# Kernel optimization log

Hardware: AMD Instinct MI355X
Metric: run time of the kernel (lower is better)

## Reference

```python
import jax, jax.numpy as jnp
import numpy as np

B, S, D_IN, D_OUT = 4, 2048, 1024, 1024

def setup_inputs() -> dict:
    key = jax.random.key(0)
    ks = jax.random.split(key, 6)
    s = 1.0 / np.sqrt(D_IN)
    return {
        "inputs": jax.random.normal(ks[0], (B, S, D_IN), dtype=jnp.float32),
        "Wq": jax.random.normal(ks[1], (D_IN, D_OUT), dtype=jnp.float32) * s,
        "Wk": jax.random.normal(ks[2], (D_IN, D_OUT), dtype=jnp.float32) * s,
        "Wv": jax.random.normal(ks[3], (D_IN, D_OUT), dtype=jnp.float32) * s,
        "Wo": jax.random.normal(ks[4], (D_OUT, D_OUT), dtype=jnp.float32) * (1.0 / np.sqrt(D_OUT)),
        "bo": jax.random.normal(ks[5], (D_OUT,), dtype=jnp.float32) * 0.01,
    }

def reference(inputs, Wq, Wk, Wv, Wo, bo):
    # QKV projections (no bias, matching qkv_bias=False)
    q = inputs @ Wq  # [B,S,D]
    k = inputs @ Wk
    v = inputs @ Wv
    # naive full attention: scores [B,S,S]
    scores = jnp.einsum('bqd,bkd->bqk', q, k) / jnp.sqrt(jnp.asarray(k.shape[-1], q.dtype))
    attn = jax.nn.softmax(scores, axis=-1)
    out = jnp.einsum('bqk,bkd->bqd', attn, v)
    return out @ Wo + bo
```

## Files before the change

kernel.cpp:

```cpp
#include <hip/hip_runtime.h>
#include <hip/hip_bf16.h>
#include <cstdint>

typedef __attribute__((ext_vector_type(8))) __bf16 bf16x8;
typedef __attribute__((ext_vector_type(4))) float  f32x4;

__device__ __forceinline__ unsigned short f2bf(float x) {
    union { float f; unsigned u; } v; v.f = x;
    unsigned r = v.u + 0x7fffu + ((v.u >> 16) & 1u);
    return (unsigned short)(r >> 16);
}
__device__ __forceinline__ unsigned pack2bf(float a, float b) {
    return (unsigned)f2bf(a) | ((unsigned)f2bf(b) << 16);
}

__device__ __forceinline__ void gld_lds16(const unsigned short* g, unsigned short* l) {
    __builtin_amdgcn_global_load_lds(
        (const __attribute__((address_space(1))) unsigned int*)g,
        (__attribute__((address_space(3))) unsigned int*)l,
        16, 0, 0);
}

__global__ void cvt_kernel(const float* __restrict__ in, unsigned short* __restrict__ out, int n4) {
    int i = blockIdx.x * blockDim.x + threadIdx.x;
    if (i < n4) {
        float4 f = ((const float4*)in)[i];
        ushort4 o;
        o.x = f2bf(f.x); o.y = f2bf(f.y); o.z = f2bf(f.z); o.w = f2bf(f.w);
        ((ushort4*)out)[i] = o;
    }
}

__global__ void wpack_kernel(const float* __restrict__ W, unsigned short* __restrict__ out) {
    int tid  = threadIdx.x;
    int lane = tid & 63;
    int chunk = blockIdx.x * 4 + (tid >> 6);
    int nt = chunk >> 5, k32 = chunk & 31;
    int r = lane & 15, q = lane >> 4;
    const float* src = W + (size_t)(k32*32 + q*8) * 1024 + nt*16 + r;
    unsigned o[4];
#pragma unroll
    for (int i = 0; i < 4; i++)
        o[i] = pack2bf(src[(size_t)(2*i) * 1024], src[(size_t)(2*i+1) * 1024]);
    *(uint4*)(out + (size_t)chunk * 512 + lane * 8) = make_uint4(o[0], o[1], o[2], o[3]);
}

__global__ void softmax_kernel(unsigned short* __restrict__ S) {
    const size_t row = blockIdx.x;
    unsigned short* p = S + row * 2048;
    const int tid = threadIdx.x;
    const int wave = tid >> 6, lane = tid & 63;

    uint4 raw = ((const uint4*)p)[tid];
    unsigned u[4] = {raw.x, raw.y, raw.z, raw.w};
    float x[8];
#pragma unroll
    for (int i = 0; i < 4; i++) {
        x[2*i]   = __uint_as_float(u[i] << 16);
        x[2*i+1] = __uint_as_float(u[i] & 0xffff0000u);
    }
    float m = x[0];
#pragma unroll
    for (int i = 1; i < 8; i++) m = fmaxf(m, x[i]);
#pragma unroll
    for (int off = 32; off >= 1; off >>= 1) m = fmaxf(m, __shfl_xor(m, off, 64));
    __shared__ float sm[4], ss[4];
    if (lane == 0) sm[wave] = m;
    __syncthreads();
    m = fmaxf(fmaxf(sm[0], sm[1]), fmaxf(sm[2], sm[3]));

    float e[8], s = 0.f;
#pragma unroll
    for (int i = 0; i < 8; i++) { e[i] = __expf(x[i] - m); s += e[i]; }
#pragma unroll
    for (int off = 32; off >= 1; off >>= 1) s += __shfl_xor(s, off, 64);
    if (lane == 0) ss[wave] = s;
    __syncthreads();
    s = ss[0] + ss[1] + ss[2] + ss[3];
    float inv = 1.0f / s;

    unsigned o[4];
#pragma unroll
    for (int i = 0; i < 4; i++)
        o[i] = pack2bf(e[2*i] * inv, e[2*i+1] * inv);
    ((uint4*)p)[tid] = make_uint4(o[0], o[1], o[2], o[3]);
}

template<int EPI>
__global__ __launch_bounds__(256)
void gemm_pk(const unsigned short* __restrict__ A, const unsigned short* __restrict__ Bpk,
             void* __restrict__ C, unsigned short* __restrict__ Ck, unsigned short* __restrict__ Cv,
             const float* __restrict__ bias,
             int lda, int ldc, int KS, int nk2, float scale,
             long long sA, long long sB, long long sC)
{
    constexpr int SMEM = (EPI == 2) ? 34816 : ((EPI == 1) ? 17408 : 16384);
    __shared__ __align__(16) char smem[SMEM];
    unsigned short* As = (unsigned short*)smem;

    const int tid  = threadIdx.x;
    const int lane = tid & 63;
    const int wave = tid >> 6;
    const int bz = blockIdx.z;
    A   += (size_t)bz * sA;
    Bpk += (size_t)bz * sB;
    const int bm = blockIdx.y * 128;
    const int bn = blockIdx.x * 128;

    const int srow = tid >> 2;
    const int scol = ((tid & 3) ^ ((tid >> 3) & 3)) * 8;
    const unsigned short* pa0 = A + (size_t)(bm + srow) * lda + scol;
    const unsigned short* pa1 = pa0 + 32;
    const unsigned short* pa2 = A + (size_t)(bm + 64 + srow) * lda + scol;
    const unsigned short* pa3 = pa2 + 32;

    const int wm = (wave & 1) * 64;
    const int wn = (wave >> 1) * 64;
    const int ln15 = lane & 15;
    const int quad = lane >> 4;
    const int fko = (quad ^ ((ln15 >> 1) & 3)) * 8;

    const unsigned short* pb[4];
#pragma unroll
    for (int j = 0; j < 4; j++)
        pb[j] = Bpk + (size_t)(((bn + wn + j*16) >> 4) * KS) * 512 + lane * 8;

    f32x4 acc[4][4];
#pragma unroll
    for (int i = 0; i < 4; i++)
#pragma unroll
        for (int j = 0; j < 4; j++) acc[i][j] = (f32x4){0.f, 0.f, 0.f, 0.f};

    const int ldsoff = tid * 16;

    for (int kt = 0; kt < nk2; ++kt) {
        __syncthreads();
        gld_lds16(pa0, (unsigned short*)(smem + ldsoff));
        gld_lds16(pa2, (unsigned short*)(smem + 4096  + ldsoff));
        gld_lds16(pa1, (unsigned short*)(smem + 8192  + ldsoff));
        gld_lds16(pa3, (unsigned short*)(smem + 12288 + ldsoff));
        pa0 += 64; pa1 += 64; pa2 += 64; pa3 += 64;
        bf16x8 b0[4], b1[4];
#pragma unroll
        for (int j = 0; j < 4; j++) {
            b0[j] = *(const bf16x8*)(pb[j]);
            b1[j] = *(const bf16x8*)(pb[j] + 512);
            pb[j] += 1024;
        }
        asm volatile("s_waitcnt vmcnt(0)" ::: "memory");
        __syncthreads();

#pragma unroll
        for (int t = 0; t < 2; t++) {
            bf16x8 af[4];
#pragma unroll
            for (int i = 0; i < 4; i++)
                af[i] = *(const bf16x8*)&As[t*4096 + (wm + i*16 + ln15) * 32 + fko];
#pragma unroll
            for (int i = 0; i < 4; i++)
#pragma unroll
                for (int j = 0; j < 4; j++)
                    acc[i][j] = __builtin_amdgcn_mfma_f32_16x16x32_bf16(
                        af[i], t ? b1[j] : b0[j], acc[i][j], 0, 0, 0);
        }
    }

    if (EPI == 0) {
        float bval[4];
#pragma unroll
        for (int j = 0; j < 4; j++) bval[j] = bias[bn + wn + j*16 + ln15];
        float* Co = (float*)C + (size_t)bz * sC;
#pragma unroll
        for (int i = 0; i < 4; i++) {
            int r0 = bm + wm + i*16 + quad*4;
#pragma unroll
            for (int j = 0; j < 4; j++) {
                int c = bn + wn + j*16 + ln15;
#pragma unroll
                for (int r = 0; r < 4; r++)
                    Co[(size_t)(r0 + r) * ldc + c] = acc[i][j][r] * scale + bval[j];
            }
        }
    } else if (EPI == 1) {
        __syncthreads();
        float* ep = (float*)(smem + wave * 4352);
        unsigned short* Co = (unsigned short*)C + (size_t)bz * sC;
#pragma unroll
        for (int i = 0; i < 4; i++) {
#pragma unroll
            for (int j = 0; j < 4; j++)
#pragma unroll
                for (int r = 0; r < 4; r++)
                    ep[(quad*4 + r) * 68 + j*16 + ln15] = acc[i][j][r] * scale;
            __builtin_amdgcn_s_waitcnt(0);
#pragma unroll
            for (int p = 0; p < 2; p++) {
                int lrow = p*8 + (lane >> 3);
                int col0 = (lane & 7) * 8;
                float4 lo = *(const float4*)&ep[lrow * 68 + col0];
                float4 hi = *(const float4*)&ep[lrow * 68 + col0 + 4];
                uint4 o;
                o.x = pack2bf(lo.x, lo.y); o.y = pack2bf(lo.z, lo.w);
                o.z = pack2bf(hi.x, hi.y); o.w = pack2bf(hi.z, hi.w);
                *(uint4*)&Co[(size_t)(bm + wm + i*16 + lrow) * ldc + bn + wn + col0] = o;
            }
            __builtin_amdgcn_s_waitcnt(0);
        }
    } else {
        __syncthreads();
        float* ep = (float*)(smem + wave * 8704);
        const int region = bn >> 10;
#pragma unroll
        for (int half = 0; half < 2; half++) {
#pragma unroll
            for (int ii = 0; ii < 2; ii++) {
                int i = half*2 + ii;
#pragma unroll
                for (int j = 0; j < 4; j++)
#pragma unroll
                    for (int r = 0; r < 4; r++)
                        ep[(ii*16 + quad*4 + r) * 68 + j*16 + ln15] = acc[i][j][r] * scale;
            }
            __builtin_amdgcn_s_waitcnt(0);
            const int mrow0 = bm + wm + half*32;
            if (region == 0) {
                unsigned short* Q = (unsigned short*)C;
#pragma unroll
                for (int p = 0; p < 4; p++) {
                    int lrow = p*8 + (lane >> 3);
                    int col0 = (lane & 7) * 8;
                    float4 lo = *(const float4*)&ep[lrow * 68 + col0];
                    float4 hi = *(const float4*)&ep[lrow * 68 + col0 + 4];
                    uint4 o;
                    o.x = pack2bf(lo.x, lo.y); o.y = pack2bf(lo.z, lo.w);
                    o.z = pack2bf(hi.x, hi.y); o.w = pack2bf(hi.z, hi.w);
                    *(uint4*)&Q[(size_t)(mrow0 + lrow) * ldc + bn + wn + col0] = o;
                }
            } else if (region == 1) {
#pragma unroll
                for (int mt = 0; mt < 2; mt++)
#pragma unroll
                    for (int c = 0; c < 2; c++) {
                        float4 f0 = *(const float4*)&ep[(mt*16 + ln15) * 68 + c*32 + quad*8];
                        float4 f1 = *(const float4*)&ep[(mt*16 + ln15) * 68 + c*32 + quad*8 + 4];
                        uint4 o;
                        o.x = pack2bf(f0.x, f0.y); o.y = pack2bf(f0.z, f0.w);
                        o.z = pack2bf(f1.x, f1.y); o.w = pack2bf(f1.z, f1.w);
                        int cid = ((mrow0 + mt*16) >> 4) * 32 + ((bn - 1024 + wn + c*32) >> 5);
                        *(uint4*)(Ck + (size_t)cid * 512 + lane * 8) = o;
                    }
            } else {
                int s32 = mrow0 >> 5;
#pragma unroll
                for (int dt = 0; dt < 4; dt++) {
                    float v[8];
#pragma unroll
                    for (int e = 0; e < 8; e++)
                        v[e] = ep[(quad*8 + e) * 68 + dt*16 + ln15];
                    uint4 o;
                    o.x = pack2bf(v[0], v[1]); o.y = pack2bf(v[2], v[3]);
                    o.z = pack2bf(v[4], v[5]); o.w = pack2bf(v[6], v[7]);
                    int cid = (((bn - 2048 + wn) >> 4) + dt) * 256 + s32;
                    *(uint4*)(Cv + (size_t)cid * 512 + lane * 8) = o;
                }
            }
            __builtin_amdgcn_s_waitcnt(0);
        }
    }
}

extern "C" void kernel_launch(void* const* d_in, const int* in_sizes, int n_in,
                              void* d_out, int out_size, void* d_ws, size_t ws_size,
                              hipStream_t stream) {
    const float* X  = (const float*)d_in[0];
    const float* Wq = (const float*)d_in[1];
    const float* Wk = (const float*)d_in[2];
    const float* Wv = (const float*)d_in[3];
    const float* Wo = (const float*)d_in[4];
    const float* bo = (const float*)d_in[5];
    float* out = (float*)d_out;

    size_t off = 0;
    auto alloc = [&](size_t bytes) {
        void* p = (char*)d_ws + off;
        off += (bytes + 255) & ~(size_t)255;
        return p;
    };
    unsigned short* Xbf  = (unsigned short*)alloc(8192ull * 1024 * 2);
    unsigned short* Wpk  = (unsigned short*)alloc(192ull * 32 * 512 * 2);
    unsigned short* Wopk = (unsigned short*)alloc(64ull * 32 * 512 * 2);
    unsigned short* Qrm  = (unsigned short*)alloc(8192ull * 1024 * 2);
    unsigned short* Kpk  = (unsigned short*)alloc(512ull * 32 * 512 * 2);
    unsigned short* Vpk  = (unsigned short*)alloc(64ull * 256 * 512 * 2);
    unsigned short* Sc   = (unsigned short*)alloc(4ull * 2048 * 2048 * 2);
    unsigned short* AO   = Xbf;

    cvt_kernel<<<(8192*1024/4 + 255)/256, 256, 0, stream>>>(X, Xbf, 8192*1024/4);
    wpack_kernel<<<512, 256, 0, stream>>>(Wq, Wpk);
    wpack_kernel<<<512, 256, 0, stream>>>(Wk, Wpk + 64*32*512);
    wpack_kernel<<<512, 256, 0, stream>>>(Wv, Wpk + 128*32*512);
    wpack_kernel<<<512, 256, 0, stream>>>(Wo, Wopk);

    gemm_pk<2><<<dim3(3072/128, 8192/128, 1), 256, 0, stream>>>(
        Xbf, Wpk, Qrm, Kpk, Vpk, nullptr, 1024, 1024, 32, 16, 1.0f, 0, 0, 0);

    gemm_pk<1><<<dim3(2048/128, 2048/128, 4), 256, 0, stream>>>(
        Qrm, Kpk, Sc, nullptr, nullptr, nullptr, 1024, 2048, 32, 16, 0.03125f,
        2048ll*1024, 128ll*32*512, 2048ll*2048);

    softmax_kernel<<<8192, 256, 0, stream>>>(Sc);

    gemm_pk<1><<<dim3(1024/128, 2048/128, 4), 256, 0, stream>>>(
        Sc, Vpk, AO, nullptr, nullptr, nullptr, 2048, 1024, 256, 32, 1.0f,
        2048ll*2048, 64ll*512, 2048ll*1024);

    gemm_pk<0><<<dim3(1024/128, 8192/128, 1), 256, 0, stream>>>(
        AO, Wopk, out, nullptr, nullptr, bo, 1024, 1024, 32, 16, 1.0f, 0, 0, 0);

    (void)n_in; (void)in_sizes; (void)out_size; (void)ws_size;
}
```

Baseline: 308.5 us.

## Double-buffer GEMM LDS tiles and B registers to overlap loads with MFMA

Rewrites the GEMM main loop as a two-stage ping-pong pipeline. The next A tile is issued into a second LDS buffer and the next B fragments into a second register set while MFMAs run on the current stage. This targets the global-load latency exposed by the old load-wait-compute loop. In exchange it doubles LDS use (32 KB for EPI 0/1), adds registers that may cut occupancy, and the kt+=2 unrolling assumes nk2 is even. The EPI 2 LDS size stays 34816, which may not fit two 16 KB stages plus its extra epilogue region.

```diff
diff --git a/kernel.cpp b/kernel.cpp
--- a/kernel.cpp
+++ b/kernel.cpp
@@ -94,9 +94,8 @@
              int lda, int ldc, int KS, int nk2, float scale,
              long long sA, long long sB, long long sC)
 {
-    constexpr int SMEM = (EPI == 2) ? 34816 : ((EPI == 1) ? 17408 : 16384);
+    constexpr int SMEM = (EPI == 2) ? 34816 : 32768;
     __shared__ __align__(16) char smem[SMEM];
-    unsigned short* As = (unsigned short*)smem;
 
     const int tid  = threadIdx.x;
     const int lane = tid & 63;
@@ -119,6 +118,7 @@
     const int ln15 = lane & 15;
     const int quad = lane >> 4;
     const int fko = (quad ^ ((ln15 >> 1) & 3)) * 8;
+    const int ldsoff = tid * 16;
 
     const unsigned short* pb[4];
 #pragma unroll
@@ -131,38 +131,48 @@
 #pragma unroll
         for (int j = 0; j < 4; j++) acc[i][j] = (f32x4){0.f, 0.f, 0.f, 0.f};
 
-    const int ldsoff = tid * 16;
-
-    for (int kt = 0; kt < nk2; ++kt) {
-        __syncthreads();
-        gld_lds16(pa0, (unsigned short*)(smem + ldsoff));
-        gld_lds16(pa2, (unsigned short*)(smem + 4096  + ldsoff));
-        gld_lds16(pa1, (unsigned short*)(smem + 8192  + ldsoff));
-        gld_lds16(pa3, (unsigned short*)(smem + 12288 + ldsoff));
+    auto stage_issue = [&](int p, bf16x8* br) {
+        char* base = smem + p * 16384;
+        gld_lds16(pa0, (unsigned short*)(base + ldsoff));
+        gld_lds16(pa2, (unsigned short*)(base + 4096  + ldsoff));
+        gld_lds16(pa1, (unsigned short*)(base + 8192  + ldsoff));
+        gld_lds16(pa3, (unsigned short*)(base + 12288 + ldsoff));
         pa0 += 64; pa1 += 64; pa2 += 64; pa3 += 64;
-        bf16x8 b0[4], b1[4];
 #pragma unroll
         for (int j = 0; j < 4; j++) {
-            b0[j] = *(const bf16x8*)(pb[j]);
-            b1[j] = *(const bf16x8*)(pb[j] + 512);
+            br[j]     = *(const bf16x8*)(pb[j]);
+            br[4 + j] = *(const bf16x8*)(pb[j] + 512);
             pb[j] += 1024;
         }
+    };
+    auto stage_compute = [&](int p, const bf16x8* br) {
+        const unsigned short* As = (const unsigned short*)(smem + p * 16384);
+#pragma unroll
+        for (int t = 0; t < 2; t++) {
+            bf16x8 af[4];
+#pragma unroll
+            for (int i = 0; i < 4; i++)
+                af[i] = *(const bf16x8*)&As[t*4096 + (wm + i*16 + ln15) * 32 + fko];
+#pragma unroll
+            for (int i = 0; i < 4; i++)
+#pragma unroll
+                for (int j = 0; j < 4; j++)
+                    acc[i][j] = __builtin_amdgcn_mfma_f32_16x16x32_bf16(
+                        af[i], br[t*4 + j], acc[i][j], 0, 0, 0);
+        }
+    };
+
+    bf16x8 b0[8], b1[8];
+    stage_issue(0, b0);
+    for (int kt = 0; kt < nk2; kt += 2) {
         asm volatile("s_waitcnt vmcnt(0)" ::: "memory");
         __syncthreads();
-
-#pragma unroll
-        for (int t = 0; t < 2; t++) {
-            bf16x8 af[4];
-#pragma unroll
-            for (int i = 0; i < 4; i++)
-                af[i] = *(const bf16x8*)&As[t*4096 + (wm + i*16 + ln15) * 32 + fko];
-#pragma unroll
-            for (int i = 0; i < 4; i++)
-#pragma unroll
-                for (int j = 0; j < 4; j++)
-                    acc[i][j] = __builtin_amdgcn_mfma_f32_16x16x32_bf16(
-                        af[i], t ? b1[j] : b0[j], acc[i][j], 0, 0, 0);
-        }
+        stage_issue(1, b1);
+        stage_compute(0, b0);
+        asm volatile("s_waitcnt vmcnt(0)" ::: "memory");
+        __syncthreads();
+        if (kt + 2 < nk2) stage_issue(0, b0);
+        stage_compute(1, b1);
     }
 
     if (EPI == 0) {
```

Measured after the change: 306.1 us. About the same (-0.8%).
